# Performance work log

Measured on AMD Instinct MI355X. Metric: run time of the kernel, lower is better.

## Reference

```python
import jax, jax.numpy as jnp
import numpy as np

B, G, T, D = 512, 10, 100, 50
H, EMB, NEMB, OUT = 30, 20, 10, 10


def _gru_last_hidden(x, W_ih, W_hh, b_ih, b_hh):
    """PyTorch-convention GRU over x:[N,T,D]; returns final hidden [N,H].
    Gate order in the 3H dim is (r, z, n), matching torch.nn.GRU."""
    N = x.shape[0]
    # precompute input projections for all timesteps: [N,T,3H] -> [T,N,3H]
    xw = jnp.einsum('ntd,gd->ntg', x, W_ih) + b_ih
    xw = jnp.swapaxes(xw, 0, 1)
    h0 = jnp.zeros((N, H), dtype=x.dtype)

    def step(h, xw_t):
        gh = h @ W_hh.T + b_hh                      # [N,3H]
        r = jax.nn.sigmoid(xw_t[:, :H] + gh[:, :H])
        z = jax.nn.sigmoid(xw_t[:, H:2 * H] + gh[:, H:2 * H])
        n = jnp.tanh(xw_t[:, 2 * H:] + r * gh[:, 2 * H:])
        h = (1.0 - z) * n + z * h
        return h, None

    hT, _ = jax.lax.scan(step, h0, xw)
    return hT


def setup_inputs() -> dict:
    key = jax.random.key(0)
    ks = jax.random.split(key, 12)
    s_g = 1.0 / np.sqrt(H)
    inp = {
        'input1': jax.random.normal(ks[0], (B, G, T, D), jnp.float32),
        'input2': jax.random.normal(ks[1], (B, G, T, D), jnp.float32),
        'W_ih': jax.random.normal(ks[2], (3 * H, D), jnp.float32) * s_g,
        'W_hh': jax.random.normal(ks[3], (3 * H, H), jnp.float32) * s_g,
        'b_ih': jax.random.normal(ks[4], (3 * H,), jnp.float32) * s_g,
        'b_hh': jax.random.normal(ks[5], (3 * H,), jnp.float32) * s_g,
        'W1': jax.random.normal(ks[6], (EMB, H * G), jnp.float32) / np.sqrt(H * G),
        'b1': jax.random.normal(ks[7], (EMB,), jnp.float32) * 0.01,
        'W2': jax.random.normal(ks[8], (NEMB, EMB), jnp.float32) / np.sqrt(EMB),
        'b2': jax.random.normal(ks[9], (NEMB,), jnp.float32) * 0.01,
        'W3': jax.random.normal(ks[10], (OUT, NEMB), jnp.float32) / np.sqrt(NEMB),
        'b3': jax.random.normal(ks[11], (OUT,), jnp.float32) * 0.01,
    }
    return inp


def reference(input1, input2, W_ih, W_hh, b_ih, b_hh, W1, b1, W2, b2, W3, b3):
    gelu = lambda v: jax.nn.gelu(v, approximate=False)  # torch GELU default = exact
    # Fuse all num_gru slices of both inputs into one big batched GRU call
    x = jnp.concatenate([input1, input2], axis=0).reshape(2 * B * G, T, D)
    hT = _gru_last_hidden(x, W_ih, W_hh, b_ih, b_hh)    # [2BG, H]
    h = hT.reshape(2, B, G * H)                          # cat over num_gru == reshape
    embeddings1, embeddings2 = h[0], h[1]               # random_dis, MLP input
    logit_emb = gelu(embeddings2 @ W1.T + b1) @ W2.T + b2
    logit = gelu(logit_emb) @ W3.T + b3
    return logit, embeddings1
```

## Files before the change

kernel.cpp:

```cpp
#include <hip/hip_runtime.h>
#include <hip/hip_bf16.h>
#include <math.h>

#define T_    100
#define D_    50
#define H_    30
#define HALF  5120
#define EMB_  20
#define NEMB_ 10
#define OUT_  10

typedef _Float16 h2    __attribute__((ext_vector_type(2)));
typedef _Float16 f16x8 __attribute__((ext_vector_type(8)));
typedef float    f32x4 __attribute__((ext_vector_type(4)));

union FR  { f16x8 v; h2 p[4]; float4 f4; };

__device__ __forceinline__ h2 pk(float a, float b) {
    return __builtin_bit_cast(h2, __builtin_amdgcn_cvt_pkrtz(a, b));
}
__device__ __forceinline__ int pki(float a, float b) {
    return __builtin_bit_cast(int, __builtin_amdgcn_cvt_pkrtz(a, b));
}

#if __has_builtin(__builtin_amdgcn_exp2f)
#define EXP2(x) __builtin_amdgcn_exp2f(x)
#else
#define EXP2(x) exp2f(x)
#endif

struct XR { float2 a0, a1, a2, a3, b0, b1, b2, b3; };

__device__ __forceinline__ int rho(int j) {
    return (j & 3) + 4 * (j >> 3) + 16 * ((j >> 2) & 1);
}

__global__ __launch_bounds__(128, 1) void gru_kernel(
    const float* __restrict__ input1, const float* __restrict__ input2,
    const float* __restrict__ W_ih,  const float* __restrict__ W_hh,
    const float* __restrict__ b_ih,  const float* __restrict__ b_hh,
    float* __restrict__ emb1_out,
    float* __restrict__ h2_out)
{
    const int tid  = threadIdx.x;
    const int lane = tid & 63;
    const int wv   = tid >> 6;
    const int s    = lane & 15;
    const int q    = lane >> 4;
    const int n    = blockIdx.x * 16 + s;

    __shared__ __align__(16) _Float16 Wst [96 * 64];
    __shared__ __align__(16) _Float16 Whst[96 * 32];
    __shared__ __align__(8)  int2     Hx[2][2][64];

    const float SC_RZ = -1.4426950408889634f;
    const float SC_N  =  2.8853900817779268f;

    for (int i = tid; i < 1536; i += 128) ((unsigned long long*)Wst)[i]  = 0ull;
    for (int i = tid; i < 768;  i += 128) ((unsigned long long*)Whst)[i] = 0ull;
    __syncthreads();

    for (int i = 0; i < 36; ++i) {
        int idx = tid + i * 128;
        if (idx < 4500) {
            int rw = idx / 50, k = idx - rw * 50;
            int g  = rw / 30,  j = rw - g * 30;
            int ge = g * 32 + rho(j);
            float sc = (g < 2) ? SC_RZ : SC_N;
            Wst[ge * 64 + k] = (_Float16)(W_ih[idx] * sc);
        }
    }
    if (tid < 90) {
        int g = tid / 30, j = tid - g * 30;
        int ge = g * 32 + rho(j);
        float sc = (g < 2) ? SC_RZ : SC_N;
        Wst[ge * 64 + 50] = (_Float16)(b_ih[tid] * sc);
    }
    for (int i = 0; i < 22; ++i) {
        int idx = tid + i * 128;
        if (idx < 2700) {
            int rw = idx / 30, k = idx - rw * 30;
            int g  = rw / 30,  j = rw - g * 30;
            int ge = g * 32 + rho(j);
            float sc = (g < 2) ? SC_RZ : SC_N;
            Whst[ge * 32 + k] = (_Float16)(W_hh[idx] * sc);
        }
    }
    if (tid < 90) {
        int g = tid / 30, j = tid - g * 30;
        int ge = g * 32 + rho(j);
        float sc = (g < 2) ? SC_RZ : SC_N;
        Whst[ge * 32 + 30] = (_Float16)(b_hh[tid] * sc);
    }
    __syncthreads();

    const int tR = wv, tZ = 2 + wv, tN = 4 + wv;
    FR wihR0, wihR1, wihZ0, wihZ1, wihN0, wihN1, whhR, whhZ, whhN;
    wihR0.f4 = *(const float4*)&Wst [(tR * 16 + s) * 64 + q * 8];
    wihR1.f4 = *(const float4*)&Wst [(tR * 16 + s) * 64 + 32 + q * 8];
    wihZ0.f4 = *(const float4*)&Wst [(tZ * 16 + s) * 64 + q * 8];
    wihZ1.f4 = *(const float4*)&Wst [(tZ * 16 + s) * 64 + 32 + q * 8];
    wihN0.f4 = *(const float4*)&Wst [(tN * 16 + s) * 64 + q * 8];
    wihN1.f4 = *(const float4*)&Wst [(tN * 16 + s) * 64 + 32 + q * 8];
    whhR.f4  = *(const float4*)&Whst[(tR * 16 + s) * 32 + q * 8];
    whhZ.f4  = *(const float4*)&Whst[(tZ * 16 + s) * 32 + q * 8];
    whhN.f4  = *(const float4*)&Whst[(tN * 16 + s) * 32 + q * 8];

    const float* xp = (n < HALF) ? input1 + (size_t)n * (T_ * D_)
                                 : input2 + (size_t)(n - HALF) * (T_ * D_);

    auto load_x = [&](int t, XR& X) {
        const float* r  = xp + t * D_;
        const float* pa = r + q * 8;
        const float* pb = (q < 2) ? (r + 32 + q * 8) : r;
        const float* p0 = (q == 2) ? (r + 48) : pb;
        X.a0 = *(const float2*)(pa + 0);
        X.a1 = *(const float2*)(pa + 2);
        X.a2 = *(const float2*)(pa + 4);
        X.a3 = *(const float2*)(pa + 6);
        X.b0 = *(const float2*)(p0);
        X.b1 = *(const float2*)(pb + 2);
        X.b2 = *(const float2*)(pb + 4);
        X.b3 = *(const float2*)(pb + 6);
    };
    auto build = [&](const XR& X, FR& x0, FR& x1) {
        x0.p[0] = pk(X.a0.x, X.a0.y); x0.p[1] = pk(X.a1.x, X.a1.y);
        x0.p[2] = pk(X.a2.x, X.a2.y); x0.p[3] = pk(X.a3.x, X.a3.y);
        if (q < 2) {
            x1.p[0] = pk(X.b0.x, X.b0.y); x1.p[1] = pk(X.b1.x, X.b1.y);
            x1.p[2] = pk(X.b2.x, X.b2.y); x1.p[3] = pk(X.b3.x, X.b3.y);
        } else if (q == 2) {
            x1.p[0] = pk(X.b0.x, X.b0.y); x1.p[1] = pk(1.f, 0.f);
            x1.p[2] = pk(0.f, 0.f);       x1.p[3] = pk(0.f, 0.f);
        } else {
            x1.p[0] = pk(0.f, 0.f); x1.p[1] = pk(0.f, 0.f);
            x1.p[2] = pk(0.f, 0.f); x1.p[3] = pk(0.f, 0.f);
        }
    };

    float hold[4] = {0.f, 0.f, 0.f, 0.f};
    int2 mine   = {0, 0};
    int2 theirs = {0, 0};
    const int ONE  = pki(1.f, 0.f);
    const int hidx = s * 4 + q;

    auto xphase = [&](XR& X, int tload, f32x4 (&xacc)[3]) {
        FR x0, x1;
        build(X, x0, x1);
        load_x(tload, X);
        f32x4 zz = {0.f, 0.f, 0.f, 0.f};
        f32x4 a;
        a = __builtin_amdgcn_mfma_f32_16x16x32_f16(wihR0.v, x0.v, zz, 0, 0, 0);
        xacc[0] = __builtin_amdgcn_mfma_f32_16x16x32_f16(wihR1.v, x1.v, a, 0, 0, 0);
        a = __builtin_amdgcn_mfma_f32_16x16x32_f16(wihZ0.v, x0.v, zz, 0, 0, 0);
        xacc[1] = __builtin_amdgcn_mfma_f32_16x16x32_f16(wihZ1.v, x1.v, a, 0, 0, 0);
        a = __builtin_amdgcn_mfma_f32_16x16x32_f16(wihN0.v, x0.v, zz, 0, 0, 0);
        xacc[2] = __builtin_amdgcn_mfma_f32_16x16x32_f16(wihN1.v, x1.v, a, 0, 0, 0);
    };
    auto step_h = [&](const f32x4 (&xacc)[3], f32x4& ar, f32x4& az, f32x4& anh) {
        const int p0 = wv ? theirs.x : mine.x;
        const int p1 = wv ? theirs.y : mine.y;
        const int p2 = wv ? mine.x   : theirs.x;
        const int p3 = wv ? mine.y   : theirs.y;
        FR bh;
        bh.p[0] = __builtin_bit_cast(h2, p0);
        bh.p[1] = __builtin_bit_cast(h2, p1);
        bh.p[2] = __builtin_bit_cast(h2, p2);
        bh.p[3] = __builtin_bit_cast(h2, q == 3 ? ONE : p3);
        f32x4 zz = {0.f, 0.f, 0.f, 0.f};
        ar  = __builtin_amdgcn_mfma_f32_16x16x32_f16(whhR.v, bh.v, xacc[0], 0, 0, 0);
        az  = __builtin_amdgcn_mfma_f32_16x16x32_f16(whhZ.v, bh.v, xacc[1], 0, 0, 0);
        anh = __builtin_amdgcn_mfma_f32_16x16x32_f16(whhN.v, bh.v, zz,      0, 0, 0);
    };
    auto step_fin = [&](const f32x4& ar, const f32x4& az, const f32x4& anh,
                        const f32x4& anx) {
        #pragma unroll
        for (int r = 0; r < 4; ++r) {
            const float er = EXP2(ar[r]);
            const float rg = __builtin_amdgcn_rcpf(1.f + er);
            const float ez = EXP2(az[r]);
            const float aa = fmaf(rg, anh[r], anx[r]);
            const float et = EXP2(aa);
            const float oz = 1.f + ez, ot = 1.f + et;
            const float ip = __builtin_amdgcn_rcpf(oz * ot);
            const float zg = ot * ip;
            const float th = fmaf(-2.f * oz, ip, 1.f);
            hold[r] = fmaf(zg, hold[r] - th, th);
        }
        mine.x = pki(hold[0], hold[1]);
        mine.y = pki(hold[2], hold[3]);
    };
    auto exchange = [&](int par) {
        Hx[par][wv][hidx] = mine;
        asm volatile("s_waitcnt lgkmcnt(0)" ::: "memory");
        __builtin_amdgcn_s_barrier();
        __builtin_amdgcn_sched_barrier(0);
        theirs = Hx[par][wv ^ 1][hidx];
    };

    XR X0, X1, X2, X3;
    load_x(0, X0); load_x(1, X1); load_x(2, X2); load_x(3, X3);
    f32x4 xaccA[3], xaccB[3];
    {
        FR x0, x1;
        build(X0, x0, x1);
        load_x(4, X0);
        f32x4 zz = {0.f, 0.f, 0.f, 0.f};
        f32x4 a;
        a = __builtin_amdgcn_mfma_f32_16x16x32_f16(wihR0.v, x0.v, zz, 0, 0, 0);
        xaccA[0] = __builtin_amdgcn_mfma_f32_16x16x32_f16(wihR1.v, x1.v, a, 0, 0, 0);
        a = __builtin_amdgcn_mfma_f32_16x16x32_f16(wihZ0.v, x0.v, zz, 0, 0, 0);
        xaccA[1] = __builtin_amdgcn_mfma_f32_16x16x32_f16(wihZ1.v, x1.v, a, 0, 0, 0);
        a = __builtin_amdgcn_mfma_f32_16x16x32_f16(wihN0.v, x0.v, zz, 0, 0, 0);
        xaccA[2] = __builtin_amdgcn_mfma_f32_16x16x32_f16(wihN1.v, x1.v, a, 0, 0, 0);
    }

    #pragma unroll 1
    for (int k = 0; k < 25; ++k) {
        const int t = 4 * k;
        f32x4 ar, az, anh;
        step_h(xaccA, ar, az, anh);
        xphase(X1, (t + 5 < 100 ? t + 5 : 99), xaccB);
        step_fin(ar, az, anh, xaccA[2]);
        exchange(0);
        step_h(xaccB, ar, az, anh);
        xphase(X2, (t + 6 < 100 ? t + 6 : 99), xaccA);
        step_fin(ar, az, anh, xaccB[2]);
        exchange(1);
        step_h(xaccA, ar, az, anh);
        xphase(X3, (t + 7 < 100 ? t + 7 : 99), xaccB);
        step_fin(ar, az, anh, xaccA[2]);
        exchange(0);
        step_h(xaccB, ar, az, anh);
        xphase(X0, (t + 8 < 100 ? t + 8 : 99), xaccA);
        step_fin(ar, az, anh, xaccB[2]);
        exchange(1);
    }

    float* outp = (n < HALF) ? emb1_out + (size_t)n * H_
                             : h2_out + (size_t)(n - HALF) * H_;
    #pragma unroll
    for (int r = 0; r < 4; ++r) {
        const int j = 8 * q + 4 * wv + r;
        if (j < H_) outp[j] = hold[r];
    }
}

__global__ __launch_bounds__(64) void mlp_kernel(
    const float* __restrict__ h2i,
    const float* __restrict__ W1, const float* __restrict__ b1,
    const float* __restrict__ W2, const float* __restrict__ b2,
    const float* __restrict__ W3, const float* __restrict__ b3,
    float* __restrict__ logit)
{
    const int b    = blockIdx.x;
    const int lane = threadIdx.x;
    __shared__ float e2[300];
    const float* row = h2i + (size_t)b * 300;
    #pragma unroll
    for (int i = lane; i < 75; i += 64)
        *(float4*)&e2[i * 4] = *(const float4*)(row + i * 4);
    __syncthreads();

    const float kInvSqrt2 = 0.70710678118654752f;
    float y1 = 0.f;
    if (lane < EMB_) {
        float acc = b1[lane];
        const float* wp = W1 + lane * 300;
        #pragma unroll
        for (int qq = 0; qq < 75; ++qq) {
            float4 wv = *(const float4*)(wp + qq * 4);
            acc += wv.x * e2[qq*4 + 0] + wv.y * e2[qq*4 + 1]
                 + wv.z * e2[qq*4 + 2] + wv.w * e2[qq*4 + 3];
        }
        y1 = 0.5f * acc * (1.f + erff(acc * kInvSqrt2));
    }
    float acc2 = (lane < NEMB_) ? b2[lane] : 0.f;
    #pragma unroll
    for (int e = 0; e < EMB_; ++e) {
        const float v = __shfl(y1, e);
        if (lane < NEMB_) acc2 += v * W2[lane * EMB_ + e];
    }
    const float y2 = 0.5f * acc2 * (1.f + erff(acc2 * kInvSqrt2));
    float acc3 = (lane < OUT_) ? b3[lane] : 0.f;
    #pragma unroll
    for (int e = 0; e < NEMB_; ++e) {
        const float v = __shfl(y2, e);
        if (lane < OUT_) acc3 += v * W3[lane * NEMB_ + e];
    }
    if (lane < OUT_) logit[(size_t)b * OUT_ + lane] = acc3;
}

extern "C" void kernel_launch(void* const* d_in, const int* in_sizes, int n_in,
                              void* d_out, int out_size, void* d_ws, size_t ws_size,
                              hipStream_t stream) {
    const float* input1 = (const float*)d_in[0];
    const float* input2 = (const float*)d_in[1];
    const float* W_ih   = (const float*)d_in[2];
    const float* W_hh   = (const float*)d_in[3];
    const float* b_ih   = (const float*)d_in[4];
    const float* b_hh   = (const float*)d_in[5];
    const float* W1     = (const float*)d_in[6];
    const float* b1     = (const float*)d_in[7];
    const float* W2     = (const float*)d_in[8];
    const float* b2     = (const float*)d_in[9];
    const float* W3     = (const float*)d_in[10];
    const float* b3     = (const float*)d_in[11];

    float* out = (float*)d_out;
    float* h2s = (float*)d_ws;

    hipLaunchKernelGGL(gru_kernel, dim3(640), dim3(128), 0, stream,
                       input1, input2, W_ih, W_hh, b_ih, b_hh,
                       out + 5120, h2s);
    hipLaunchKernelGGL(mlp_kernel, dim3(512), dim3(64), 0, stream,
                       h2s, W1, b1, W2, b2, W3, b3, out);
}
```

Measured before the change: 96.79 us.

## Alternate split and redundant full GRU steps to halve cross-wave barriers

```diff
diff --git a/kernel.cpp b/kernel.cpp
--- a/kernel.cpp
+++ b/kernel.cpp
@@ -94,17 +94,13 @@
     }
     __syncthreads();
 
-    const int tR = wv, tZ = 2 + wv, tN = 4 + wv;
-    FR wihR0, wihR1, wihZ0, wihZ1, wihN0, wihN1, whhR, whhZ, whhN;
-    wihR0.f4 = *(const float4*)&Wst [(tR * 16 + s) * 64 + q * 8];
-    wihR1.f4 = *(const float4*)&Wst [(tR * 16 + s) * 64 + 32 + q * 8];
-    wihZ0.f4 = *(const float4*)&Wst [(tZ * 16 + s) * 64 + q * 8];
-    wihZ1.f4 = *(const float4*)&Wst [(tZ * 16 + s) * 64 + 32 + q * 8];
-    wihN0.f4 = *(const float4*)&Wst [(tN * 16 + s) * 64 + q * 8];
-    wihN1.f4 = *(const float4*)&Wst [(tN * 16 + s) * 64 + 32 + q * 8];
-    whhR.f4  = *(const float4*)&Whst[(tR * 16 + s) * 32 + q * 8];
-    whhZ.f4  = *(const float4*)&Whst[(tZ * 16 + s) * 32 + q * 8];
-    whhN.f4  = *(const float4*)&Whst[(tN * 16 + s) * 32 + q * 8];
+    FR wih[6][2], whh[6];
+    #pragma unroll
+    for (int nt = 0; nt < 6; ++nt) {
+        wih[nt][0].f4 = *(const float4*)&Wst [(nt * 16 + s) * 64 + q * 8];
+        wih[nt][1].f4 = *(const float4*)&Wst [(nt * 16 + s) * 64 + 32 + q * 8];
+        whh[nt].f4    = *(const float4*)&Whst[(nt * 16 + s) * 32 + q * 8];
+    }
 
     const float* xp = (n < HALF) ? input1 + (size_t)n * (T_ * D_)
                                  : input2 + (size_t)(n - HALF) * (T_ * D_);
@@ -138,26 +134,13 @@
         }
     };
 
-    float hold[4] = {0.f, 0.f, 0.f, 0.f};
+    float hold8[8] = {0.f, 0.f, 0.f, 0.f, 0.f, 0.f, 0.f, 0.f};
     int2 mine   = {0, 0};
     int2 theirs = {0, 0};
     const int ONE  = pki(1.f, 0.f);
     const int hidx = s * 4 + q;
 
-    auto xphase = [&](XR& X, int tload, f32x4 (&xacc)[3]) {
-        FR x0, x1;
-        build(X, x0, x1);
-        load_x(tload, X);
-        f32x4 zz = {0.f, 0.f, 0.f, 0.f};
-        f32x4 a;
-        a = __builtin_amdgcn_mfma_f32_16x16x32_f16(wihR0.v, x0.v, zz, 0, 0, 0);
-        xacc[0] = __builtin_amdgcn_mfma_f32_16x16x32_f16(wihR1.v, x1.v, a, 0, 0, 0);
-        a = __builtin_amdgcn_mfma_f32_16x16x32_f16(wihZ0.v, x0.v, zz, 0, 0, 0);
-        xacc[1] = __builtin_amdgcn_mfma_f32_16x16x32_f16(wihZ1.v, x1.v, a, 0, 0, 0);
-        a = __builtin_amdgcn_mfma_f32_16x16x32_f16(wihN0.v, x0.v, zz, 0, 0, 0);
-        xacc[2] = __builtin_amdgcn_mfma_f32_16x16x32_f16(wihN1.v, x1.v, a, 0, 0, 0);
-    };
-    auto step_h = [&](const f32x4 (&xacc)[3], f32x4& ar, f32x4& az, f32x4& anh) {
+    auto make_bh = [&]() -> FR {
         const int p0 = wv ? theirs.x : mine.x;
         const int p1 = wv ? theirs.y : mine.y;
         const int p2 = wv ? mine.x   : theirs.x;
@@ -167,74 +150,128 @@
         bh.p[1] = __builtin_bit_cast(h2, p1);
         bh.p[2] = __builtin_bit_cast(h2, p2);
         bh.p[3] = __builtin_bit_cast(h2, q == 3 ? ONE : p3);
+        return bh;
+    };
+
+    auto xphase_full = [&](XR& X, int tload, f32x4 (&xaccF)[6]) {
+        FR x0, x1;
+        build(X, x0, x1);
+        load_x(tload, X);
+        #pragma unroll
+        for (int i = 0; i < 6; ++i) {
+            f32x4 zz = {0.f, 0.f, 0.f, 0.f};
+            f32x4 a = __builtin_amdgcn_mfma_f32_16x16x32_f16(wih[i][0].v, x0.v, zz, 0, 0, 0);
+            xaccF[i] = __builtin_amdgcn_mfma_f32_16x16x32_f16(wih[i][1].v, x1.v, a, 0, 0, 0);
+        }
+    };
+    auto xphase_split = [&](XR& X, int tload, f32x4 (&xaccS)[3]) {
+        FR x0, x1;
+        build(X, x0, x1);
+        load_x(tload, X);
         f32x4 zz = {0.f, 0.f, 0.f, 0.f};
-        ar  = __builtin_amdgcn_mfma_f32_16x16x32_f16(whhR.v, bh.v, xacc[0], 0, 0, 0);
-        az  = __builtin_amdgcn_mfma_f32_16x16x32_f16(whhZ.v, bh.v, xacc[1], 0, 0, 0);
-        anh = __builtin_amdgcn_mfma_f32_16x16x32_f16(whhN.v, bh.v, zz,      0, 0, 0);
-    };
-    auto step_fin = [&](const f32x4& ar, const f32x4& az, const f32x4& anh,
-                        const f32x4& anx) {
+        f32x4 a;
+        a = __builtin_amdgcn_mfma_f32_16x16x32_f16(wih[wv][0].v,     x0.v, zz, 0, 0, 0);
+        xaccS[0] = __builtin_amdgcn_mfma_f32_16x16x32_f16(wih[wv][1].v,     x1.v, a, 0, 0, 0);
+        a = __builtin_amdgcn_mfma_f32_16x16x32_f16(wih[2 + wv][0].v, x0.v, zz, 0, 0, 0);
+        xaccS[1] = __builtin_amdgcn_mfma_f32_16x16x32_f16(wih[2 + wv][1].v, x1.v, a, 0, 0, 0);
+        a = __builtin_amdgcn_mfma_f32_16x16x32_f16(wih[4 + wv][0].v, x0.v, zz, 0, 0, 0);
+        xaccS[2] = __builtin_amdgcn_mfma_f32_16x16x32_f16(wih[4 + wv][1].v, x1.v, a, 0, 0, 0);
+    };
+
+    auto split_step = [&](const f32x4 (&xaccS)[3], int par) {
+        FR bh = make_bh();
+        f32x4 zz = {0.f, 0.f, 0.f, 0.f};
+        f32x4 ar  = __builtin_amdgcn_mfma_f32_16x16x32_f16(whh[wv].v,     bh.v, xaccS[0], 0, 0, 0);
+        f32x4 az  = __builtin_amdgcn_mfma_f32_16x16x32_f16(whh[2 + wv].v, bh.v, xaccS[1], 0, 0, 0);
+        f32x4 anh = __builtin_amdgcn_mfma_f32_16x16x32_f16(whh[4 + wv].v, bh.v, zz,       0, 0, 0);
         #pragma unroll
         for (int r = 0; r < 4; ++r) {
             const float er = EXP2(ar[r]);
             const float rg = __builtin_amdgcn_rcpf(1.f + er);
             const float ez = EXP2(az[r]);
-            const float aa = fmaf(rg, anh[r], anx[r]);
+            const float aa = fmaf(rg, anh[r], xaccS[2][r]);
             const float et = EXP2(aa);
             const float oz = 1.f + ez, ot = 1.f + et;
             const float ip = __builtin_amdgcn_rcpf(oz * ot);
             const float zg = ot * ip;
             const float th = fmaf(-2.f * oz, ip, 1.f);
-            hold[r] = fmaf(zg, hold[r] - th, th);
-        }
-        mine.x = pki(hold[0], hold[1]);
-        mine.y = pki(hold[2], hold[3]);
-    };
-    auto exchange = [&](int par) {
+            hold8[wv * 4 + r] = fmaf(zg, hold8[wv * 4 + r] - th, th);
+        }
+        mine.x = pki(hold8[wv * 4 + 0], hold8[wv * 4 + 1]);
+        mine.y = pki(hold8[wv * 4 + 2], hold8[wv * 4 + 3]);
         Hx[par][wv][hidx] = mine;
         asm volatile("s_waitcnt lgkmcnt(0)" ::: "memory");
         __builtin_amdgcn_s_barrier();
         __builtin_amdgcn_sched_barrier(0);
         theirs = Hx[par][wv ^ 1][hidx];
+        h2 t0 = __builtin_bit_cast(h2, theirs.x);
+        h2 t1 = __builtin_bit_cast(h2, theirs.y);
+        const int pb = (wv ^ 1) * 4;
+        hold8[pb + 0] = (float)t0[0]; hold8[pb + 1] = (float)t0[1];
+        hold8[pb + 2] = (float)t1[0]; hold8[pb + 3] = (float)t1[1];
+    };
+
+    auto full_step = [&](const f32x4 (&xaccF)[6]) {
+        FR bh = make_bh();
+        f32x4 arz[4], ah[2];
+        #pragma unroll
+        for (int nt = 0; nt < 4; ++nt)
+            arz[nt] = __builtin_amdgcn_mfma_f32_16x16x32_f16(whh[nt].v, bh.v, xaccF[nt], 0, 0, 0);
+        #pragma unroll
+        for (int u = 0; u < 2; ++u) {
+            f32x4 zz = {0.f, 0.f, 0.f, 0.f};
+            ah[u] = __builtin_amdgcn_mfma_f32_16x16x32_f16(whh[4 + u].v, bh.v, zz, 0, 0, 0);
+        }
+        #pragma unroll
+        for (int u = 0; u < 2; ++u) {
+            #pragma unroll
+            for (int r = 0; r < 4; ++r) {
+                const float er = EXP2(arz[u][r]);
+                const float rg = __builtin_amdgcn_rcpf(1.f + er);
+                const float ez = EXP2(arz[2 + u][r]);
+                const float aa = fmaf(rg, ah[u][r], xaccF[4 + u][r]);
+                const float et = EXP2(aa);
+                const float oz = 1.f + ez, ot = 1.f + et;
+                const float ip = __builtin_amdgcn_rcpf(oz * ot);
+                const float zg = ot * ip;
+                const float th = fmaf(-2.f * oz, ip, 1.f);
+                hold8[u * 4 + r] = fmaf(zg, hold8[u * 4 + r] - th, th);
+            }
+        }
+        mine.x   = pki(hold8[wv * 4 + 0],       hold8[wv * 4 + 1]);
+        mine.y   = pki(hold8[wv * 4 + 2],       hold8[wv * 4 + 3]);
+        theirs.x = pki(hold8[(wv ^ 1) * 4 + 0], hold8[(wv ^ 1) * 4 + 1]);
+        theirs.y = pki(hold8[(wv ^ 1) * 4 + 2], hold8[(wv ^ 1) * 4 + 3]);
     };
 
     XR X0, X1, X2, X3;
     load_x(0, X0); load_x(1, X1); load_x(2, X2); load_x(3, X3);
-    f32x4 xaccA[3], xaccB[3];
+    f32x4 xaccS[3], xaccF[6];
     {
         FR x0, x1;
         build(X0, x0, x1);
         load_x(4, X0);
         f32x4 zz = {0.f, 0.f, 0.f, 0.f};
         f32x4 a;
-        a = __builtin_amdgcn_mfma_f32_16x16x32_f16(wihR0.v, x0.v, zz, 0, 0, 0);
-        xaccA[0] = __builtin_amdgcn_mfma_f32_16x16x32_f16(wihR1.v, x1.v, a, 0, 0, 0);
-        a = __builtin_amdgcn_mfma_f32_16x16x32_f16(wihZ0.v, x0.v, zz, 0, 0, 0);
-        xaccA[1] = __builtin_amdgcn_mfma_f32_16x16x32_f16(wihZ1.v, x1.v, a, 0, 0, 0);
-        a = __builtin_amdgcn_mfma_f32_16x16x32_f16(wihN0.v, x0.v, zz, 0, 0, 0);
-        xaccA[2] = __builtin_amdgcn_mfma_f32_16x16x32_f16(wihN1.v, x1.v, a, 0, 0, 0);
+        a = __builtin_amdgcn_mfma_f32_16x16x32_f16(wih[wv][0].v,     x0.v, zz, 0, 0, 0);
+        xaccS[0] = __builtin_amdgcn_mfma_f32_16x16x32_f16(wih[wv][1].v,     x1.v, a, 0, 0, 0);
+        a = __builtin_amdgcn_mfma_f32_16x16x32_f16(wih[2 + wv][0].v, x0.v, zz, 0, 0, 0);
+        xaccS[1] = __builtin_amdgcn_mfma_f32_16x16x32_f16(wih[2 + wv][1].v, x1.v, a, 0, 0, 0);
+        a = __builtin_amdgcn_mfma_f32_16x16x32_f16(wih[4 + wv][0].v, x0.v, zz, 0, 0, 0);
+        xaccS[2] = __builtin_amdgcn_mfma_f32_16x16x32_f16(wih[4 + wv][1].v, x1.v, a, 0, 0, 0);
     }
 
     #pragma unroll 1
     for (int k = 0; k < 25; ++k) {
         const int t = 4 * k;
-        f32x4 ar, az, anh;
-        step_h(xaccA, ar, az, anh);
-        xphase(X1, (t + 5 < 100 ? t + 5 : 99), xaccB);
-        step_fin(ar, az, anh, xaccA[2]);
-        exchange(0);
-        step_h(xaccB, ar, az, anh);
-        xphase(X2, (t + 6 < 100 ? t + 6 : 99), xaccA);
-        step_fin(ar, az, anh, xaccB[2]);
-        exchange(1);
-        step_h(xaccA, ar, az, anh);
-        xphase(X3, (t + 7 < 100 ? t + 7 : 99), xaccB);
-        step_fin(ar, az, anh, xaccA[2]);
-        exchange(0);
-        step_h(xaccB, ar, az, anh);
-        xphase(X0, (t + 8 < 100 ? t + 8 : 99), xaccA);
-        step_fin(ar, az, anh, xaccB[2]);
-        exchange(1);
+        xphase_full(X1, (t + 5 < 100 ? t + 5 : 99), xaccF);
+        split_step(xaccS, 0);
+        xphase_split(X2, (t + 6 < 100 ? t + 6 : 99), xaccS);
+        full_step(xaccF);
+        xphase_full(X3, (t + 7 < 100 ? t + 7 : 99), xaccF);
+        split_step(xaccS, 1);
+        xphase_split(X0, (t + 8 < 100 ? t + 8 : 99), xaccS);
+        full_step(xaccF);
     }
 
     float* outp = (n < HALF) ? emb1_out + (size_t)n * H_
@@ -242,7 +279,7 @@
     #pragma unroll
     for (int r = 0; r < 4; ++r) {
         const int j = 8 * q + 4 * wv + r;
-        if (j < H_) outp[j] = hold[r];
+        if (j < H_) outp[j] = hold8[wv * 4 + r];
     }
 }
 
```

Result: slower. 248.2 us (+156.4%).
